# Optimization experiments

Measured on AMD Instinct MI355X. Metric: run time of the kernel, lower is better.

The kernel has to match this reference:

```python
import jax, jax.numpy as jnp
import numpy as np

N_NODES = 50000
N_EDGES = 800000
IN_CH = 128
HIDDEN = 32
HEADS = 4
NEG_SLOPE = 0.2


def segment_softmax(e, seg, num_segments):
    # numerically stable softmax over edges grouped by destination node
    m = jax.ops.segment_max(e, seg, num_segments=num_segments)
    ex = jnp.exp(e - m[seg])
    denom = jax.ops.segment_sum(ex, seg, num_segments=num_segments)
    return ex / denom[seg]


def gat_layer(x, src, dst, W, a_src, a_dst, b, num_nodes, concat):
    H, C = a_src.shape
    h = (x @ W).reshape(num_nodes, H, C)            # (N, H, C)
    alpha_s = jnp.einsum('nhc,hc->nh', h, a_src)    # (N, H)
    alpha_d = jnp.einsum('nhc,hc->nh', h, a_dst)    # (N, H)
    e = jax.nn.leaky_relu(alpha_s[src] + alpha_d[dst], negative_slope=NEG_SLOPE)  # (E, H)
    att = segment_softmax(e, dst, num_nodes)        # (E, H)
    out = jax.ops.segment_sum(h[src] * att[:, :, None], dst, num_segments=num_nodes)  # (N, H, C)
    if concat:
        out = out.reshape(num_nodes, H * C)
    else:
        out = out.mean(axis=1)
    return out + b


def setup_inputs() -> dict:
    key = jax.random.key(0)
    ks = jax.random.split(key, 12)
    s = 0.1
    return {
        'x': jax.random.normal(ks[0], (N_NODES, IN_CH), dtype=jnp.float32),
        'edge_index': jax.random.randint(ks[1], (2, N_EDGES), 0, N_NODES, dtype=jnp.int64),
        'W1': jax.random.normal(ks[2], (IN_CH, HEADS * HIDDEN), dtype=jnp.float32) * s,
        'a_src1': jax.random.normal(ks[3], (HEADS, HIDDEN), dtype=jnp.float32) * s,
        'a_dst1': jax.random.normal(ks[4], (HEADS, HIDDEN), dtype=jnp.float32) * s,
        'b1': jnp.zeros((HEADS * HIDDEN,), dtype=jnp.float32),
        'W2': jax.random.normal(ks[5], (HEADS * HIDDEN, 1 * HIDDEN), dtype=jnp.float32) * s,
        'a_src2': jax.random.normal(ks[6], (1, HIDDEN), dtype=jnp.float32) * s,
        'a_dst2': jax.random.normal(ks[7], (1, HIDDEN), dtype=jnp.float32) * s,
        'b2': jnp.zeros((HIDDEN,), dtype=jnp.float32),
    }


def reference(x, edge_index, W1, a_src1, a_dst1, b1, W2, a_src2, a_dst2, b2):
    n = x.shape[0]
    loops = jnp.arange(n, dtype=edge_index.dtype)
    src = jnp.concatenate([edge_index[0], loops])  # PyG GATConv add_self_loops=True
    dst = jnp.concatenate([edge_index[1], loops])
    h = gat_layer(x, src, dst, W1, a_src1, a_dst1, b1, n, concat=True)
    h = jax.nn.elu(h)  # ELU between layers (dropout=0.0)
    out = gat_layer(h, src, dst, W2, a_src2, a_dst2, b2, n, concat=False)
    return out
```

## Files before the change

### kernel.cpp

```cpp
#include <hip/hip_runtime.h>
#include <cstdint>

#define NEG_SLOPE 0.2f
#define LDA 136
#define PB  256
#define CAP 5120
#define SMEM_BYTES (64 * LDA * 2)

__device__ __forceinline__ float leaky(float v) { return v > 0.f ? v : NEG_SLOPE * v; }
__device__ __forceinline__ float elu(float v) { return v > 0.f ? v : __expf(v) - 1.f; }

typedef _Float16 half2v __attribute__((ext_vector_type(2)));
typedef _Float16 f16x8 __attribute__((ext_vector_type(8)));
typedef float f32x4 __attribute__((ext_vector_type(4)));
union H8 { float4 f4; half2v h[4]; f16x8 v8; };
union H4 { float2 f2; half2v h[2]; };
union HF2 { float2 f2; _Float16 h[4]; };
union HH { f16x8 v; half2v h[4]; };


__device__ __forceinline__ void prep_body(int bid, int G, int tid,
        const float* __restrict__ W1, const float* __restrict__ W2,
        _Float16* __restrict__ W1t, _Float16* __restrict__ W2t) {
    for (int i = bid * 256 + tid; i < 128 * 128; i += G * 256) {
        int c = i >> 7, k = i & 127;
        W1t[i] = (_Float16)W1[k * 128 + c];
    }
    for (int i = bid * 256 + tid; i < 32 * 128; i += G * 256) {
        int c = i >> 7, k = i & 127;
        W2t[i] = (_Float16)W2[k * 32 + c];
    }
}

__device__ __forceinline__ void gemm1_tile(int b, int tid, _Float16* Ah,
        const float* __restrict__ x, const _Float16* __restrict__ W1t,
        const float* __restrict__ a_src, const float* __restrict__ a_dst,
        _Float16* __restrict__ h1h, float* __restrict__ as1, float* __restrict__ ad1,
        int n) {
    int row0 = b * 64;
    const float4* x4 = (const float4*)x;
#pragma unroll
    for (int i = 0; i < 8; ++i) {
        int idx = tid + i * 256;
        int row = idx >> 5, c4 = idx & 31;
        float4 v = make_float4(0.f, 0.f, 0.f, 0.f);
        if (row0 + row < n) v = x4[(size_t)(row0 + row) * 32 + c4];
        HF2 u;
        u.h[0] = (_Float16)v.x; u.h[1] = (_Float16)v.y;
        u.h[2] = (_Float16)v.z; u.h[3] = (_Float16)v.w;
        *(float2*)&Ah[row * LDA + c4 * 4] = u.f2;
    }
    __syncthreads();

    int l = tid & 63, w = tid >> 6;
    int lr = l & 15, lg = l >> 4;
    f16x8 af[4];
#pragma unroll
    for (int kk = 0; kk < 4; ++kk)
        af[kk] = *(const f16x8*)&Ah[(w * 16 + lr) * LDA + kk * 32 + lg * 8];
    f32x4 acc[8];
#pragma unroll
    for (int t = 0; t < 8; ++t) acc[t] = (f32x4)0.f;
#pragma unroll
    for (int t = 0; t < 8; ++t) {
#pragma unroll
        for (int kk = 0; kk < 4; ++kk) {
            f16x8 bf = *(const f16x8*)&W1t[(size_t)(t * 16 + lr) * 128 + kk * 32 + lg * 8];
            acc[t] = __builtin_amdgcn_mfma_f32_16x16x32_f16(af[kk], bf, acc[t], 0, 0, 0);
        }
    }
    __syncthreads();
#pragma unroll
    for (int t = 0; t < 8; ++t)
#pragma unroll
        for (int r = 0; r < 4; ++r)
            Ah[(w * 16 + lg * 4 + r) * LDA + t * 16 + lr] = (_Float16)acc[t][r];
    __syncthreads();
    int row = tid >> 2, q = tid & 3;
    if (row0 + row < n) {
        const float* asv = a_src + q * 32;
        const float* adv = a_dst + q * 32;
        float ps = 0.f, pd = 0.f;
#pragma unroll
        for (int j = 0; j < 4; ++j) {
            f16x8 v = *(const f16x8*)&Ah[row * LDA + q * 32 + j * 8];
            *(f16x8*)&h1h[(size_t)(row0 + row) * 128 + q * 32 + j * 8] = v;
#pragma unroll
            for (int e = 0; e < 8; ++e) {
                float f = (float)v[e];
                ps += f * asv[j * 8 + e];
                pd += f * adv[j * 8 + e];
            }
        }
        as1[(row0 + row) * 4 + q] = ps;
        ad1[(row0 + row) * 4 + q] = pd;
    }
}


__global__ __launch_bounds__(256) void pairprep_kernel(
        const int* __restrict__ src, const int* __restrict__ dstp,
        int* __restrict__ bcur, int2* __restrict__ pairs,
        int E, int NB, int CH,
        const float* __restrict__ W1, const float* __restrict__ W2,
        _Float16* __restrict__ W1t, _Float16* __restrict__ W2t) {
    int bid = (int)blockIdx.x, tid = threadIdx.x;
    if (bid >= PB) {
        prep_body(bid - PB, (int)gridDim.x - PB, tid, W1, W2, W1t, W2t);
        return;
    }
    __shared__ int lh[256];
    for (int t = tid; t < NB; t += 256) lh[t] = 0;
    __syncthreads();
    int e0 = bid * CH, e1 = min(e0 + CH, E);
    int nv = (e1 - e0) & ~3;
    for (int i = e0 + tid * 4; i < e0 + nv; i += 1024) {
        int4 d = *(const int4*)(dstp + i);
        atomicAdd(&lh[d.x >> 8], 1);
        atomicAdd(&lh[d.y >> 8], 1);
        atomicAdd(&lh[d.z >> 8], 1);
        atomicAdd(&lh[d.w >> 8], 1);
    }
    for (int i = e0 + nv + tid; i < e1; i += 256)
        atomicAdd(&lh[dstp[i] >> 8], 1);
    __syncthreads();
    for (int t = tid; t < NB; t += 256) {
        int c = lh[t];
        lh[t] = (c > 0) ? atomicAdd(&bcur[t], c) : 0;
    }
    __syncthreads();
    for (int i = e0 + tid * 4; i < e0 + nv; i += 1024) {
        int4 d = *(const int4*)(dstp + i);
        int4 s = *(const int4*)(src + i);
        int b0 = d.x >> 8, b1 = d.y >> 8, b2 = d.z >> 8, b3 = d.w >> 8;
        int r0 = atomicAdd(&lh[b0], 1);
        int r1 = atomicAdd(&lh[b1], 1);
        int r2 = atomicAdd(&lh[b2], 1);
        int r3 = atomicAdd(&lh[b3], 1);
        if (r0 < CAP) pairs[(size_t)b0 * CAP + r0] = make_int2(s.x, d.x & 255);
        if (r1 < CAP) pairs[(size_t)b1 * CAP + r1] = make_int2(s.y, d.y & 255);
        if (r2 < CAP) pairs[(size_t)b2 * CAP + r2] = make_int2(s.z, d.z & 255);
        if (r3 < CAP) pairs[(size_t)b3 * CAP + r3] = make_int2(s.w, d.w & 255);
    }
    for (int i = e0 + nv + tid; i < e1; i += 256) {
        int d = dstp[i];
        int b = d >> 8;
        int r = atomicAdd(&lh[b], 1);
        if (r < CAP) pairs[(size_t)b * CAP + r] = make_int2(src[i], d & 255);
    }
}

__device__ __forceinline__ void csr_bucket(int b, int tid, unsigned char* smem,
        const int2* __restrict__ pairs, const int* __restrict__ bcur,
        int* __restrict__ rp, int* __restrict__ col, int E, int N, int NB) {
    int* lsz    = (int*)smem;
    int* lstart = lsz + 256;
    int* lnh    = lstart + 256;
    int* lnex   = lnh + 256;
    int* lncur  = lnex + 256;
    int* wsum   = lncur + 256;
    int* woff   = wsum + 4;
    int lane = tid & 63, wv = tid >> 6;

    lsz[tid] = (tid < NB) ? bcur[tid] : 0;
    __syncthreads();
    int v = lsz[tid];
    int x = v;
#pragma unroll
    for (int o = 1; o < 64; o <<= 1) { int u = __shfl_up(x, o); if (lane >= o) x += u; }
    if (lane == 63) wsum[wv] = x;
    __syncthreads();
    if (tid == 0) { int a = 0; for (int i = 0; i < 4; ++i) { woff[i] = a; a += wsum[i]; } }
    __syncthreads();
    lstart[tid] = x - v + woff[wv];
    __syncthreads();

    if (b >= NB) { if (tid == 0) rp[N] = E; return; }
    int myStart = lstart[b];
    int S = lsz[b]; if (S > CAP) S = CAP;
    const int2* pb = pairs + (size_t)b * CAP;

    lnh[tid] = 0;
    __syncthreads();
    for (int i = tid; i < S; i += 256) atomicAdd(&lnh[pb[i].y], 1);
    __syncthreads();
    int v2 = lnh[tid];
    int x2 = v2;
#pragma unroll
    for (int o = 1; o < 64; o <<= 1) { int u = __shfl_up(x2, o); if (lane >= o) x2 += u; }
    if (lane == 63) wsum[wv] = x2;
    __syncthreads();
    if (tid == 0) { int a = 0; for (int i = 0; i < 4; ++i) { woff[i] = a; a += wsum[i]; } }
    __syncthreads();
    int ex2 = x2 - v2 + woff[wv];
    lnex[tid] = ex2;
    lncur[tid] = 0;
    int node = (b << 8) + tid;
    if (node <= N) rp[node] = myStart + ex2;
    __syncthreads();
    for (int i = tid; i < S; i += 256) {
        int2 p = pb[i];
        int r = atomicAdd(&lncur[p.y], 1);
        col[myStart + lnex[p.y] + r] = p.x;
    }
}

__global__ __launch_bounds__(256) void csr_gemm_kernel(
        const int2* __restrict__ pairs, const int* __restrict__ bcur,
        int* __restrict__ rp, int* __restrict__ col, int E, int N, int NB, int KB,
        const float* __restrict__ x, const _Float16* __restrict__ W1t,
        const float* __restrict__ a_src, const float* __restrict__ a_dst,
        _Float16* __restrict__ h1h, float* __restrict__ as1, float* __restrict__ ad1) {
    __shared__ __align__(16) unsigned char smem[SMEM_BYTES];
    int bid = (int)blockIdx.x;
    if (bid < KB) {
        csr_bucket(bid, threadIdx.x, smem, pairs, bcur, rp, col, E, N, NB);
        return;
    }
    gemm1_tile(bid - KB, threadIdx.x, (_Float16*)smem, x, W1t, a_src, a_dst,
               h1h, as1, ad1, N);
}

#define W2S 136

__global__ __launch_bounds__(256) void agg1_kernel(const _Float16* __restrict__ h1h,
                                                   const float4* __restrict__ as1,
                                                   const float4* __restrict__ ad1,
                                                   const int* __restrict__ rp,
                                                   const int* __restrict__ col,
                                                   const float* __restrict__ b1,
                                                   const _Float16* __restrict__ W2t,
                                                   const float* __restrict__ a_src2,
                                                   const float* __restrict__ a_dst2,
                                                   _Float16* __restrict__ h2h,
                                                   float* __restrict__ as2,
                                                   float* __restrict__ ad2, int n) {
    __shared__ float4 s_p[4][64];
    __shared__ _Float16 s_row[4][2][128];
    __shared__ _Float16 sW2[32 * W2S];
    int tid = threadIdx.x;
    for (int e = tid; e < 32 * 16; e += 256) {
        int c = e >> 4, k8 = e & 15;
        *(f16x8*)&sW2[c * W2S + k8 * 8] = *(const f16x8*)&W2t[c * 128 + k8 * 8];
    }
    float a2s = a_src2[tid & 31], a2d = a_dst2[tid & 31];
    __syncthreads();

    int wave = tid >> 6, lane = tid & 63;
    int h = lane >> 5, l5 = lane & 31;
    int g = l5 & 15, sub = l5 >> 4;
    int head = g >> 2;
    int nid = blockIdx.x * 8 + wave * 2 + h;
    bool vn = nid < n;
    int nc = vn ? nid : 0;
    float4* sp = s_p[wave];
    int start = rp[nc];
    int end = vn ? rp[nc + 1] : start;
    float4 adn = ad1[nc], asn = as1[nc];
    float sv = (head == 0) ? asn.x + adn.x : (head == 1) ? asn.y + adn.y
             : (head == 2) ? asn.z + adn.z : asn.w + adn.w;
    float psf_h = vn ? __expf(leaky(sv)) : 0.f;
    float dnum = 0.f;
    float4 a0 = make_float4(0.f, 0.f, 0.f, 0.f);
    float4 a1 = a0;

    for (int base = start; base < end; base += 32) {
        int i = base + l5;
        int sidx = 0;
        float4 p = make_float4(0.f, 0.f, 0.f, 0.f);
        if (i < end) {
            sidx = col[i];
            float4 a = as1[sidx];
            p.x = __expf(leaky(a.x + adn.x));
            p.y = __expf(leaky(a.y + adn.y));
            p.z = __expf(leaky(a.z + adn.z));
            p.w = __expf(leaky(a.w + adn.w));
        }
        sp[lane] = p;
        int len = min(32, end - base);
        int steps = (len + 1) >> 1;
#pragma unroll 4
        for (int s = 0; s < steps; ++s) {
            int j = s * 2 + sub;
            bool valid = j < len;
            int js = valid ? j : 0;
            int sl = (h << 5) + js;
            int rj = __shfl(sidx, sl);
            float pj = ((const float*)&sp[sl])[head];
            pj = valid ? pj : 0.f;
            H8 u = ((const H8*)(h1h + (size_t)rj * 128))[g];
            dnum += pj;
            a0.x += (float)u.h[0].x * pj; a0.y += (float)u.h[0].y * pj;
            a0.z += (float)u.h[1].x * pj; a0.w += (float)u.h[1].y * pj;
            a1.x += (float)u.h[2].x * pj; a1.y += (float)u.h[2].y * pj;
            a1.z += (float)u.h[3].x * pj; a1.w += (float)u.h[3].y * pj;
        }
    }
    if (sub == 0) {
        H8 u = ((const H8*)(h1h + (size_t)nc * 128))[g];
        dnum += psf_h;
        a0.x += (float)u.h[0].x * psf_h; a0.y += (float)u.h[0].y * psf_h;
        a0.z += (float)u.h[1].x * psf_h; a0.w += (float)u.h[1].y * psf_h;
        a1.x += (float)u.h[2].x * psf_h; a1.y += (float)u.h[2].y * psf_h;
        a1.z += (float)u.h[3].x * psf_h; a1.w += (float)u.h[3].y * psf_h;
    }
    a0.x += __shfl_xor(a0.x, 16); a0.y += __shfl_xor(a0.y, 16);
    a0.z += __shfl_xor(a0.z, 16); a0.w += __shfl_xor(a0.w, 16);
    a1.x += __shfl_xor(a1.x, 16); a1.y += __shfl_xor(a1.y, 16);
    a1.z += __shfl_xor(a1.z, 16); a1.w += __shfl_xor(a1.w, 16);
    dnum += __shfl_xor(dnum, 16);
    if (sub == 0 && vn) {
        float inv = __builtin_amdgcn_rcpf(dnum);
        const float4* b4 = (const float4*)b1;
        float4 bb0 = b4[g * 2], bb1 = b4[g * 2 + 1];
        float4 r0 = make_float4(elu(a0.x * inv + bb0.x), elu(a0.y * inv + bb0.y),
                                elu(a0.z * inv + bb0.z), elu(a0.w * inv + bb0.w));
        float4 r1 = make_float4(elu(a1.x * inv + bb1.x), elu(a1.y * inv + bb1.y),
                                elu(a1.z * inv + bb1.z), elu(a1.w * inv + bb1.w));
        H8 o8;
        o8.h[0] = half2v{(_Float16)r0.x, (_Float16)r0.y};
        o8.h[1] = half2v{(_Float16)r0.z, (_Float16)r0.w};
        o8.h[2] = half2v{(_Float16)r1.x, (_Float16)r1.y};
        o8.h[3] = half2v{(_Float16)r1.z, (_Float16)r1.w};
        *(float4*)&s_row[wave][h][g * 8] = o8.f4;
    }
    int c = l5;
    float acc2 = 0.f;
#pragma unroll
    for (int k8 = 0; k8 < 16; ++k8) {
        HH rv, wvv;
        rv.v  = *(const f16x8*)&s_row[wave][h][k8 * 8];
        wvv.v = *(const f16x8*)&sW2[c * W2S + k8 * 8];
#if __has_builtin(__builtin_amdgcn_fdot2)
        acc2 = __builtin_amdgcn_fdot2(rv.h[0], wvv.h[0], acc2, false);
        acc2 = __builtin_amdgcn_fdot2(rv.h[1], wvv.h[1], acc2, false);
        acc2 = __builtin_amdgcn_fdot2(rv.h[2], wvv.h[2], acc2, false);
        acc2 = __builtin_amdgcn_fdot2(rv.h[3], wvv.h[3], acc2, false);
#else
#pragma unroll
        for (int e = 0; e < 8; ++e) acc2 += (float)rv.v[e] * (float)wvv.v[e];
#endif
    }
    float ps = acc2 * a2s, pd = acc2 * a2d;
#pragma unroll
    for (int o = 1; o < 32; o <<= 1) { ps += __shfl_xor(ps, o); pd += __shfl_xor(pd, o); }
    if (vn) {
        h2h[(size_t)nid * 32 + c] = (_Float16)acc2;
        if (l5 == 0) { as2[nid] = ps; ad2[nid] = pd; }
    }
}

__global__ __launch_bounds__(256) void agg2_kernel(const _Float16* __restrict__ h2h,
                                                   const float* __restrict__ as2,
                                                   const float* __restrict__ ad2,
                                                   const int* __restrict__ rp,
                                                   const int* __restrict__ col,
                                                   const float* __restrict__ b2,
                                                   float* __restrict__ out, int n) {
    int wave = threadIdx.x >> 6, lane = threadIdx.x & 63;
    int h = lane >> 5, l5 = lane & 31;
    int g = l5 & 7, sub = l5 >> 3;
    int nid = blockIdx.x * 8 + wave * 2 + h;
    bool vn = nid < n;
    int nc = vn ? nid : 0;
    int start = rp[nc];
    int end = vn ? rp[nc + 1] : start;
    float adn = ad2[nc];
    float psf = vn ? __expf(leaky(as2[nc] + adn)) : 0.f;
    float dnum = 0.f;
    float4 acc = make_float4(0.f, 0.f, 0.f, 0.f);
    for (int base = start; base < end; base += 32) {
        int i = base + l5;
        int sidx = 0;
        float p = 0.f;
        if (i < end) {
            sidx = col[i];
            p = __expf(leaky(as2[sidx] + adn));
        }
        int len = min(32, end - base);
        int steps = (len + 3) >> 2;
#pragma unroll 4
        for (int s = 0; s < steps; ++s) {
            int j = s * 4 + sub;
            bool valid = j < len;
            int js = valid ? j : 0;
            int sl = (h << 5) + js;
            int rj = __shfl(sidx, sl);
            float pj = __shfl(p, sl);
            pj = valid ? pj : 0.f;
            H4 u = ((const H4*)(h2h + (size_t)rj * 32))[g];
            dnum += pj;
            acc.x += (float)u.h[0].x * pj; acc.y += (float)u.h[0].y * pj;
            acc.z += (float)u.h[1].x * pj; acc.w += (float)u.h[1].y * pj;
        }
    }
    if (sub == 0) {
        H4 u = ((const H4*)(h2h + (size_t)nc * 32))[g];
        dnum += psf;
        acc.x += (float)u.h[0].x * psf; acc.y += (float)u.h[0].y * psf;
        acc.z += (float)u.h[1].x * psf; acc.w += (float)u.h[1].y * psf;
    }
#pragma unroll
    for (int o = 8; o < 32; o <<= 1) {
        acc.x += __shfl_xor(acc.x, o); acc.y += __shfl_xor(acc.y, o);
        acc.z += __shfl_xor(acc.z, o); acc.w += __shfl_xor(acc.w, o);
        dnum += __shfl_xor(dnum, o);
    }
    if (sub == 0 && vn) {
        float inv = __builtin_amdgcn_rcpf(dnum);
        float4 bb = ((const float4*)b2)[g];
        ((float4*)(out + (size_t)nid * 32))[g] =
            make_float4(acc.x * inv + bb.x, acc.y * inv + bb.y,
                        acc.z * inv + bb.z, acc.w * inv + bb.w);
    }
}


extern "C" void kernel_launch(void* const* d_in, const int* in_sizes, int n_in,
                              void* d_out, int out_size, void* d_ws, size_t ws_size,
                              hipStream_t stream) {
    const float* x      = (const float*)d_in[0];
    const int*   ei     = (const int*)d_in[1];
    const float* W1     = (const float*)d_in[2];
    const float* a_src1 = (const float*)d_in[3];
    const float* a_dst1 = (const float*)d_in[4];
    const float* b1     = (const float*)d_in[5];
    const float* W2     = (const float*)d_in[6];
    const float* a_src2 = (const float*)d_in[7];
    const float* a_dst2 = (const float*)d_in[8];
    const float* b2     = (const float*)d_in[9];
    float* out = (float*)d_out;

    const int N = in_sizes[0] / 128;
    const int E = in_sizes[1] / 2;
    const int* src = ei;
    const int* dstp = ei + E;

    uint8_t* w = (uint8_t*)d_ws;
    auto carve = [&](size_t bytes) {
        uint8_t* p = w;
        w += (bytes + 255) & ~(size_t)255;
        return p;
    };
    _Float16* h1h = (_Float16*)carve((size_t)N * 128 * 2);
    _Float16* h2h = (_Float16*)carve((size_t)N * 32 * 2);
    _Float16* W1t = (_Float16*)carve((size_t)128 * 128 * 2);
    _Float16* W2t = (_Float16*)carve((size_t)32 * 128 * 2);
    float* as1 = (float*)carve((size_t)N * 4 * 4);
    float* ad1 = (float*)carve((size_t)N * 4 * 4);
    float* as2 = (float*)carve((size_t)N * 4);
    float* ad2 = (float*)carve((size_t)N * 4);
    int* rp    = (int*)carve((size_t)(N + 1) * 4);
    int* col   = (int*)carve((size_t)E * 4);
    int* bcur  = (int*)carve(256 * 4);

    const int NB = ((N - 1) >> 8) + 1;
    const int KB = (N >> 8) + 1;
    int CH = (E + PB - 1) / PB;
    CH = (CH + 3) & ~3;
    const int gemmBlocks = (N + 63) / 64;
    const int aggGroups = (N + 7) / 8;

    int2* pairs = (int2*)carve((size_t)NB * CAP * 8);

    hipMemsetAsync(bcur, 0, 256 * 4, stream);
    pairprep_kernel<<<PB + 80, 256, 0, stream>>>(src, dstp, bcur, pairs,
                                                 E, NB, CH, W1, W2, W1t, W2t);
    csr_gemm_kernel<<<KB + gemmBlocks, 256, 0, stream>>>(
        pairs, bcur, rp, col, E, N, NB, KB,
        x, W1t, a_src1, a_dst1, h1h, as1, ad1);
    agg1_kernel<<<aggGroups, 256, 0, stream>>>(h1h, (const float4*)as1,
                                               (const float4*)ad1, rp, col, b1,
                                               W2t, a_src2, a_dst2, h2h, as2, ad2, N);
    agg2_kernel<<<aggGroups, 256, 0, stream>>>(h2h, as2, ad2, rp, col, b2, out, N);
}
```

Measured before the change: 189.6 us.

## Map more destination nodes per wave in both GAT aggregation kernels

Both aggregation kernels now give each destination node a 16-lane (layer 1) or 8-lane (layer 2) group instead of 32 lanes. Each wave therefore handles 4 or 8 nodes, and the neighbor loop no longer splits edges across sub-groups, which removes the cross-subgroup shuffle reductions and the masked steps. The layer-2 projection in agg1 now computes two output channels per lane. The aim is less idle lane work on short per-node edge lists (about 17 edges on average), at the cost of longer serial loops for high-degree nodes and fewer loads in flight per node.

```diff
diff --git a/kernel.cpp b/kernel.cpp
--- a/kernel.cpp
+++ b/kernel.cpp
@@ -236,21 +236,20 @@
                                                    float* __restrict__ as2,
                                                    float* __restrict__ ad2, int n) {
     __shared__ float4 s_p[4][64];
-    __shared__ _Float16 s_row[4][2][128];
+    __shared__ _Float16 s_row[4][4][128];
     __shared__ _Float16 sW2[32 * W2S];
     int tid = threadIdx.x;
     for (int e = tid; e < 32 * 16; e += 256) {
         int c = e >> 4, k8 = e & 15;
         *(f16x8*)&sW2[c * W2S + k8 * 8] = *(const f16x8*)&W2t[c * 128 + k8 * 8];
     }
-    float a2s = a_src2[tid & 31], a2d = a_dst2[tid & 31];
     __syncthreads();
 
     int wave = tid >> 6, lane = tid & 63;
-    int h = lane >> 5, l5 = lane & 31;
-    int g = l5 & 15, sub = l5 >> 4;
+    int q4 = lane >> 4, l4 = lane & 15;
+    int g = l4;
     int head = g >> 2;
-    int nid = blockIdx.x * 8 + wave * 2 + h;
+    int nid = blockIdx.x * 16 + wave * 4 + q4;
     bool vn = nid < n;
     int nc = vn ? nid : 0;
     float4* sp = s_p[wave];
@@ -264,8 +263,8 @@
     float4 a0 = make_float4(0.f, 0.f, 0.f, 0.f);
     float4 a1 = a0;
 
-    for (int base = start; base < end; base += 32) {
-        int i = base + l5;
+    for (int base = start; base < end; base += 16) {
+        int i = base + l4;
         int sidx = 0;
         float4 p = make_float4(0.f, 0.f, 0.f, 0.f);
         if (i < end) {
@@ -277,17 +276,12 @@
             p.w = __expf(leaky(a.w + adn.w));
         }
         sp[lane] = p;
-        int len = min(32, end - base);
-        int steps = (len + 1) >> 1;
+        int len = min(16, end - base);
 #pragma unroll 4
-        for (int s = 0; s < steps; ++s) {
-            int j = s * 2 + sub;
-            bool valid = j < len;
-            int js = valid ? j : 0;
-            int sl = (h << 5) + js;
+        for (int s = 0; s < len; ++s) {
+            int sl = (lane & 48) + s;
             int rj = __shfl(sidx, sl);
             float pj = ((const float*)&sp[sl])[head];
-            pj = valid ? pj : 0.f;
             H8 u = ((const H8*)(h1h + (size_t)rj * 128))[g];
             dnum += pj;
             a0.x += (float)u.h[0].x * pj; a0.y += (float)u.h[0].y * pj;
@@ -296,7 +290,7 @@
             a1.z += (float)u.h[3].x * pj; a1.w += (float)u.h[3].y * pj;
         }
     }
-    if (sub == 0) {
+    {
         H8 u = ((const H8*)(h1h + (size_t)nc * 128))[g];
         dnum += psf_h;
         a0.x += (float)u.h[0].x * psf_h; a0.y += (float)u.h[0].y * psf_h;
@@ -304,12 +298,7 @@
         a1.x += (float)u.h[2].x * psf_h; a1.y += (float)u.h[2].y * psf_h;
         a1.z += (float)u.h[3].x * psf_h; a1.w += (float)u.h[3].y * psf_h;
     }
-    a0.x += __shfl_xor(a0.x, 16); a0.y += __shfl_xor(a0.y, 16);
-    a0.z += __shfl_xor(a0.z, 16); a0.w += __shfl_xor(a0.w, 16);
-    a1.x += __shfl_xor(a1.x, 16); a1.y += __shfl_xor(a1.y, 16);
-    a1.z += __shfl_xor(a1.z, 16); a1.w += __shfl_xor(a1.w, 16);
-    dnum += __shfl_xor(dnum, 16);
-    if (sub == 0 && vn) {
+    if (vn) {
         float inv = __builtin_amdgcn_rcpf(dnum);
         const float4* b4 = (const float4*)b1;
         float4 bb0 = b4[g * 2], bb1 = b4[g * 2 + 1];
@@ -322,31 +311,41 @@
         o8.h[1] = half2v{(_Float16)r0.z, (_Float16)r0.w};
         o8.h[2] = half2v{(_Float16)r1.x, (_Float16)r1.y};
         o8.h[3] = half2v{(_Float16)r1.z, (_Float16)r1.w};
-        *(float4*)&s_row[wave][h][g * 8] = o8.f4;
-    }
-    int c = l5;
-    float acc2 = 0.f;
+        *(float4*)&s_row[wave][q4][g * 8] = o8.f4;
+    }
+    int c0 = l4, c1 = l4 + 16;
+    float acc2a = 0.f, acc2b = 0.f;
 #pragma unroll
     for (int k8 = 0; k8 < 16; ++k8) {
-        HH rv, wvv;
-        rv.v  = *(const f16x8*)&s_row[wave][h][k8 * 8];
-        wvv.v = *(const f16x8*)&sW2[c * W2S + k8 * 8];
+        HH rv, w0, w1;
+        rv.v = *(const f16x8*)&s_row[wave][q4][k8 * 8];
+        w0.v = *(const f16x8*)&sW2[c0 * W2S + k8 * 8];
+        w1.v = *(const f16x8*)&sW2[c1 * W2S + k8 * 8];
 #if __has_builtin(__builtin_amdgcn_fdot2)
-        acc2 = __builtin_amdgcn_fdot2(rv.h[0], wvv.h[0], acc2, false);
-        acc2 = __builtin_amdgcn_fdot2(rv.h[1], wvv.h[1], acc2, false);
-        acc2 = __builtin_amdgcn_fdot2(rv.h[2], wvv.h[2], acc2, false);
-        acc2 = __builtin_amdgcn_fdot2(rv.h[3], wvv.h[3], acc2, false);
+        acc2a = __builtin_amdgcn_fdot2(rv.h[0], w0.h[0], acc2a, false);
+        acc2a = __builtin_amdgcn_fdot2(rv.h[1], w0.h[1], acc2a, false);
+        acc2a = __builtin_amdgcn_fdot2(rv.h[2], w0.h[2], acc2a, false);
+        acc2a = __builtin_amdgcn_fdot2(rv.h[3], w0.h[3], acc2a, false);
+        acc2b = __builtin_amdgcn_fdot2(rv.h[0], w1.h[0], acc2b, false);
+        acc2b = __builtin_amdgcn_fdot2(rv.h[1], w1.h[1], acc2b, false);
+        acc2b = __builtin_amdgcn_fdot2(rv.h[2], w1.h[2], acc2b, false);
+        acc2b = __builtin_amdgcn_fdot2(rv.h[3], w1.h[3], acc2b, false);
 #else
 #pragma unroll
-        for (int e = 0; e < 8; ++e) acc2 += (float)rv.v[e] * (float)wvv.v[e];
+        for (int e = 0; e < 8; ++e) {
+            acc2a += (float)rv.v[e] * (float)w0.v[e];
+            acc2b += (float)rv.v[e] * (float)w1.v[e];
+        }
 #endif
     }
-    float ps = acc2 * a2s, pd = acc2 * a2d;
-#pragma unroll
-    for (int o = 1; o < 32; o <<= 1) { ps += __shfl_xor(ps, o); pd += __shfl_xor(pd, o); }
+    float ps = acc2a * a_src2[c0] + acc2b * a_src2[c1];
+    float pd = acc2a * a_dst2[c0] + acc2b * a_dst2[c1];
+#pragma unroll
+    for (int o = 1; o < 16; o <<= 1) { ps += __shfl_xor(ps, o); pd += __shfl_xor(pd, o); }
     if (vn) {
-        h2h[(size_t)nid * 32 + c] = (_Float16)acc2;
-        if (l5 == 0) { as2[nid] = ps; ad2[nid] = pd; }
+        h2h[(size_t)nid * 32 + c0] = (_Float16)acc2a;
+        h2h[(size_t)nid * 32 + c1] = (_Float16)acc2b;
+        if (l4 == 0) { as2[nid] = ps; ad2[nid] = pd; }
     }
 }
 
@@ -358,9 +357,9 @@
                                                    const float* __restrict__ b2,
                                                    float* __restrict__ out, int n) {
     int wave = threadIdx.x >> 6, lane = threadIdx.x & 63;
-    int h = lane >> 5, l5 = lane & 31;
-    int g = l5 & 7, sub = l5 >> 3;
-    int nid = blockIdx.x * 8 + wave * 2 + h;
+    int q8 = lane >> 3, l3 = lane & 7;
+    int g = l3;
+    int nid = blockIdx.x * 32 + wave * 8 + q8;
     bool vn = nid < n;
     int nc = vn ? nid : 0;
     int start = rp[nc];
@@ -369,44 +368,33 @@
     float psf = vn ? __expf(leaky(as2[nc] + adn)) : 0.f;
     float dnum = 0.f;
     float4 acc = make_float4(0.f, 0.f, 0.f, 0.f);
-    for (int base = start; base < end; base += 32) {
-        int i = base + l5;
+    for (int base = start; base < end; base += 8) {
+        int i = base + l3;
         int sidx = 0;
         float p = 0.f;
         if (i < end) {
             sidx = col[i];
             p = __expf(leaky(as2[sidx] + adn));
         }
-        int len = min(32, end - base);
-        int steps = (len + 3) >> 2;
+        int len = min(8, end - base);
 #pragma unroll 4
-        for (int s = 0; s < steps; ++s) {
-            int j = s * 4 + sub;
-            bool valid = j < len;
-            int js = valid ? j : 0;
-            int sl = (h << 5) + js;
+        for (int s = 0; s < len; ++s) {
+            int sl = (lane & 56) + s;
             int rj = __shfl(sidx, sl);
             float pj = __shfl(p, sl);
-            pj = valid ? pj : 0.f;
             H4 u = ((const H4*)(h2h + (size_t)rj * 32))[g];
             dnum += pj;
             acc.x += (float)u.h[0].x * pj; acc.y += (float)u.h[0].y * pj;
             acc.z += (float)u.h[1].x * pj; acc.w += (float)u.h[1].y * pj;
         }
     }
-    if (sub == 0) {
+    {
         H4 u = ((const H4*)(h2h + (size_t)nc * 32))[g];
         dnum += psf;
         acc.x += (float)u.h[0].x * psf; acc.y += (float)u.h[0].y * psf;
         acc.z += (float)u.h[1].x * psf; acc.w += (float)u.h[1].y * psf;
     }
-#pragma unroll
-    for (int o = 8; o < 32; o <<= 1) {
-        acc.x += __shfl_xor(acc.x, o); acc.y += __shfl_xor(acc.y, o);
-        acc.z += __shfl_xor(acc.z, o); acc.w += __shfl_xor(acc.w, o);
-        dnum += __shfl_xor(dnum, o);
-    }
-    if (sub == 0 && vn) {
+    if (vn) {
         float inv = __builtin_amdgcn_rcpf(dnum);
         float4 bb = ((const float4*)b2)[g];
         ((float4*)(out + (size_t)nid * 32))[g] =
@@ -459,7 +447,8 @@
     int CH = (E + PB - 1) / PB;
     CH = (CH + 3) & ~3;
     const int gemmBlocks = (N + 63) / 64;
-    const int aggGroups = (N + 7) / 8;
+    const int agg1Groups = (N + 15) / 16;
+    const int agg2Groups = (N + 31) / 32;
 
     int2* pairs = (int2*)carve((size_t)NB * CAP * 8);
 
@@ -469,8 +458,8 @@
     csr_gemm_kernel<<<KB + gemmBlocks, 256, 0, stream>>>(
         pairs, bcur, rp, col, E, N, NB, KB,
         x, W1t, a_src1, a_dst1, h1h, as1, ad1);
-    agg1_kernel<<<aggGroups, 256, 0, stream>>>(h1h, (const float4*)as1,
-                                               (const float4*)ad1, rp, col, b1,
-                                               W2t, a_src2, a_dst2, h2h, as2, ad2, N);
-    agg2_kernel<<<aggGroups, 256, 0, stream>>>(h2h, as2, ad2, rp, col, b2, out, N);
-}
+    agg1_kernel<<<agg1Groups, 256, 0, stream>>>(h1h, (const float4*)as1,
+                                                (const float4*)ad1, rp, col, b1,
+                                                W2t, a_src2, a_dst2, h2h, as2, ad2, N);
+    agg2_kernel<<<agg2Groups, 256, 0, stream>>>(h2h, as2, ad2, rp, col, b2, out, N);
+}
```

New measurement: 184.4 us. 2.8% less time.
